# Kernel tuning notes

Measured on AMD Instinct MI355X. Metric: run time of the kernel, lower is better.

The kernel has to match this reference:

```python
import jax, jax.numpy as jnp
import numpy as np

B, T, D, H = 4, 2048, 1024, 16
DH = D // H  # 64


def setup_inputs() -> dict:
    key = jax.random.key(0)
    k1, k2, k3 = jax.random.split(key, 3)
    x = jax.random.normal(k1, (B, T, D), dtype=jnp.float32)
    w_qkv = jax.random.normal(k2, (D, 3 * D), dtype=jnp.float32) * (D ** -0.5)
    w_out = jax.random.normal(k3, (D, D), dtype=jnp.float32) * (D ** -0.5)
    return {"x": x, "w_qkv": w_qkv, "w_out": w_out}


def reference(x, w_qkv, w_out):
    b, t, d = x.shape
    qkv = jnp.einsum('btd,de->bte', x, w_qkv)  # [B,T,3D]
    q, k, v = jnp.split(qkv, 3, axis=-1)
    # [B,H,T,DH]
    q = q.reshape(b, t, H, DH).transpose(0, 2, 1, 3)
    k = k.reshape(b, t, H, DH).transpose(0, 2, 1, 3)
    v = v.reshape(b, t, H, DH).transpose(0, 2, 1, 3)
    logits = jnp.einsum('bhqd,bhkd->bhqk', q, k) * (1.0 / jnp.sqrt(jnp.float32(DH)))
    # causal bias: -inf strictly above the diagonal (key index > query index)
    causal = jnp.tril(jnp.ones((t, t), dtype=bool))
    logits = jnp.where(causal, logits, jnp.float32(-jnp.inf))
    scores = jax.nn.softmax(logits, axis=-1)
    y = jnp.einsum('bhqk,bhkd->bhqd', scores, v)
    y = y.transpose(0, 2, 1, 3).reshape(b, t, d)
    return jnp.einsum('btd,de->bte', y, w_out)
```

## Files before the change

### kernel.cpp

```cpp
#include <hip/hip_runtime.h>
#include <hip/hip_bf16.h>


namespace {
constexpr int kB = 4, kT = 2048, kD = 1024, kH = 16;
constexpr int kM = kB * kT;
constexpr int kNq = 3 * kD;
constexpr float kS = 0.180336880f;
}

typedef unsigned short u16;
typedef short bf16x8 __attribute__((ext_vector_type(8)));
typedef float f32x4 __attribute__((ext_vector_type(4)));

__device__ __forceinline__ u16 f2bf(float f) {
  unsigned int u = __float_as_uint(f);
  u += 0x7fffu + ((u >> 16) & 1u);
  return (u16)(u >> 16);
}
__device__ __forceinline__ unsigned int pack2(float a, float b) {
  return (unsigned int)f2bf(a) | ((unsigned int)f2bf(b) << 16);
}
__device__ __forceinline__ unsigned int cvtpk(float a, float b) {
  unsigned int r;
  asm("v_cvt_pk_bf16_f32 %0, %1, %2" : "=v"(r) : "v"(a), "v"(b));
  return r;
}

__device__ __forceinline__ void gload16(const u16* g, u16* l) {
  __builtin_amdgcn_global_load_lds(
      (const __attribute__((address_space(1))) unsigned int*)(uintptr_t)g,
      (__attribute__((address_space(3))) unsigned int*)(uintptr_t)l, 16, 0, 0);
}

__global__ __launch_bounds__(256) void cvt_bf16(const float* __restrict__ x,
                                                u16* __restrict__ xb) {
  const size_t i = ((size_t)blockIdx.x * 256 + threadIdx.x) * 8;
  const float4 v0 = *(const float4*)(x + i);
  const float4 v1 = *(const float4*)(x + i + 4);
  uint4 p;
  p.x = pack2(v0.x, v0.y);
  p.y = pack2(v0.z, v0.w);
  p.z = pack2(v1.x, v1.y);
  p.w = pack2(v1.z, v1.w);
  *(uint4*)(xb + i) = p;
}

__global__ __launch_bounds__(256) void transpose_bf(const float* __restrict__ W,
                                                    u16* __restrict__ WT,
                                                    int K, int N, int nscale) {
  __shared__ float T[32][33];
  const int tid = threadIdx.x;
  const int nb = blockIdx.x * 32, kb = blockIdx.y * 32;
  const int r = tid >> 3, c = (tid & 7) * 4;
  const float4 v = *(const float4*)&W[(size_t)(kb + r) * N + nb + c];
  T[r][c + 0] = v.x;
  T[r][c + 1] = v.y;
  T[r][c + 2] = v.z;
  T[r][c + 3] = v.w;
  __syncthreads();
  const float s = (nb + r < nscale) ? kS : 1.0f;
  uint2 p;
  p.x = pack2(T[c + 0][r] * s, T[c + 1][r] * s);
  p.y = pack2(T[c + 2][r] * s, T[c + 3][r] * s);
  *(uint2*)&WT[(size_t)(nb + r) * K + kb + c] = p;
}

template <bool F32OUT>
__global__ __launch_bounds__(256) void gemm_bt(const u16* __restrict__ A,
                                               const u16* __restrict__ BT,
                                               void* __restrict__ Cv, int lda,
                                               int ldc) {
  __shared__ u16 As[128 * 32];
  __shared__ u16 Bs[128 * 32];
  const int tid = threadIdx.x;
  const int w = tid >> 6, lane = tid & 63;
  const int col = lane & 15, quad = lane >> 4;
  const int wm = (w & 1) * 64, wn = (w >> 1) * 64;
  const int m0 = blockIdx.y * 128, n0 = blockIdx.x * 128;

  const int s0 = tid, s1 = 256 + tid;
  const int ar0 = s0 >> 2, ak0 = ((s0 & 3) ^ ((ar0 >> 1) & 3)) * 8;
  const int ar1 = s1 >> 2, ak1 = ((s1 & 3) ^ ((ar1 >> 1) & 3)) * 8;
  const u16* agp0 = A + (size_t)(m0 + ar0) * lda + ak0;
  const u16* agp1 = A + (size_t)(m0 + ar1) * lda + ak1;
  const u16* bgp0 = BT + (size_t)(n0 + ar0) * kD + ak0;
  const u16* bgp1 = BT + (size_t)(n0 + ar1) * kD + ak1;
  u16* al0 = &As[s0 * 8];
  u16* al1 = &As[s1 * 8];
  u16* bl0 = &Bs[s0 * 8];
  u16* bl1 = &Bs[s1 * 8];

  f32x4 acc[4][4];
#pragma unroll
  for (int mi = 0; mi < 4; ++mi)
#pragma unroll
    for (int ni = 0; ni < 4; ++ni) acc[mi][ni] = (f32x4){0.f, 0.f, 0.f, 0.f};

  for (int k0 = 0; k0 < kD; k0 += 32) {
    __syncthreads();
    gload16(agp0 + k0, al0);
    gload16(agp1 + k0, al1);
    gload16(bgp0 + k0, bl0);
    gload16(bgp1 + k0, bl1);
    __syncthreads();
    bf16x8 af[4], bfr[4];
#pragma unroll
    for (int mi = 0; mi < 4; ++mi) {
      const int r = wm + mi * 16 + col;
      af[mi] = *(const bf16x8*)&As[r * 32 + ((quad ^ ((r >> 1) & 3)) * 8)];
    }
#pragma unroll
    for (int ni = 0; ni < 4; ++ni) {
      const int r = wn + ni * 16 + col;
      bfr[ni] = *(const bf16x8*)&Bs[r * 32 + ((quad ^ ((r >> 1) & 3)) * 8)];
    }
#pragma unroll
    for (int mi = 0; mi < 4; ++mi)
#pragma unroll
      for (int ni = 0; ni < 4; ++ni)
        acc[mi][ni] = __builtin_amdgcn_mfma_f32_16x16x32_bf16(
            af[mi], bfr[ni], acc[mi][ni], 0, 0, 0);
  }

#pragma unroll
  for (int mi = 0; mi < 4; ++mi)
#pragma unroll
    for (int reg = 0; reg < 4; ++reg) {
      const int row = m0 + wm + mi * 16 + quad * 4 + reg;
#pragma unroll
      for (int ni = 0; ni < 4; ++ni) {
        const int cc = n0 + wn + ni * 16 + col;
        if (F32OUT)
          ((float*)Cv)[(size_t)row * ldc + cc] = acc[mi][ni][reg];
        else
          ((u16*)Cv)[(size_t)row * ldc + cc] = f2bf(acc[mi][ni][reg]);
      }
    }
}

__global__ __launch_bounds__(256) void attn_fwd(u16* __restrict__ qkv) {
  __shared__ u16 Ks[64 * 64];
  __shared__ u16 Vt[64][72];
  __shared__ u16 Ps[64][72];
  const int tid = threadIdx.x;
  const int w = tid >> 6, lane = tid & 63;
  const int col = lane & 15, quad = lane >> 4;
  const int bh = blockIdx.x;
  const int b = bh >> 4, h = bh & 15;
  const int pa = blockIdx.y;
  const size_t base = (size_t)(b * kT) * kNq + h * 64;

  const int krr = lane >> 3;
  const int ksw = (lane & 7) ^ krr;
  const u16* const kgbase =
      qkv + base + kD + (size_t)(w * 16 + krr) * kNq + ksw * 8;
  u16* const kl0 = &Ks[(w * 16) * 64];
  u16* const kl1 = &Ks[(w * 16 + 8) * 64];

  const int vkp = (tid & 31) * 2, vd0 = (tid >> 5) * 8;

#pragma unroll
  for (int pass = 0; pass < 2; ++pass) {
    const int qt = pass ? (31 - pa) : pa;
    const int q0 = qt << 6;

    bf16x8 aq[2];
#pragma unroll
    for (int ks = 0; ks < 2; ++ks)
      aq[ks] = *(const bf16x8*)(qkv + base + (size_t)(q0 + w * 16 + col) * kNq +
                                ks * 32 + quad * 8);

    f32x4 o[4];
#pragma unroll
    for (int nt = 0; nt < 4; ++nt) o[nt] = (f32x4){0.f, 0.f, 0.f, 0.f};
    float l_i = 0.f;

    for (int kt = 0; kt <= qt; ++kt) {
      const int k0 = kt << 6;
      __syncthreads();
      gload16(kgbase + (size_t)k0 * kNq, kl0);
      gload16(kgbase + (size_t)(k0 + 8) * kNq, kl1);
      {
        const u16* vp = qkv + base + 2 * kD + (size_t)(k0 + vkp) * kNq + vd0;
        const uint4 va = *(const uint4*)vp;
        const uint4 vb = *(const uint4*)(vp + kNq);
        const unsigned int* aw = (const unsigned int*)&va;
        const unsigned int* bw = (const unsigned int*)&vb;
#pragma unroll
        for (int i = 0; i < 4; ++i) {
          *(unsigned int*)&Vt[vd0 + 2 * i][vkp] =
              __builtin_amdgcn_perm(bw[i], aw[i], 0x05040100u);
          *(unsigned int*)&Vt[vd0 + 2 * i + 1][vkp] =
              __builtin_amdgcn_perm(bw[i], aw[i], 0x07060302u);
        }
      }
      __syncthreads();

      f32x4 st[4];
#pragma unroll
      for (int nt = 0; nt < 4; ++nt) st[nt] = (f32x4){0.f, 0.f, 0.f, 0.f};
#pragma unroll
      for (int ks = 0; ks < 2; ++ks) {
#pragma unroll
        for (int nt = 0; nt < 4; ++nt) {
          const int kr = nt * 16 + col;
          const bf16x8 bk = *(const bf16x8*)&Ks[kr * 64 +
                                                (((ks * 4 + quad) ^ (col & 7)) *
                                                 8)];
          st[nt] = __builtin_amdgcn_mfma_f32_16x16x32_bf16(bk, aq[ks], st[nt],
                                                           0, 0, 0);
        }
      }

      float psum = 0.f;
      if (kt == qt) {
        const int qrel = w * 16 + col;
#pragma unroll
        for (int nt = 0; nt < 4; ++nt)
#pragma unroll
          for (int reg = 0; reg < 4; ++reg) {
            const int krel = nt * 16 + quad * 4 + reg;
            const float p = (krel <= qrel) ? exp2f(st[nt][reg]) : 0.f;
            st[nt][reg] = p;
            psum += p;
          }
      } else {
#pragma unroll
        for (int nt = 0; nt < 4; ++nt)
#pragma unroll
          for (int reg = 0; reg < 4; ++reg) {
            const float p = exp2f(st[nt][reg]);
            st[nt][reg] = p;
            psum += p;
          }
      }
      psum += __shfl_xor(psum, 16, 64);
      psum += __shfl_xor(psum, 32, 64);
      l_i += psum;

#pragma unroll
      for (int nt = 0; nt < 4; ++nt) {
        uint2 pk;
        pk.x = cvtpk(st[nt][0], st[nt][1]);
        pk.y = cvtpk(st[nt][2], st[nt][3]);
        *(uint2*)&Ps[w * 16 + col][nt * 16 + quad * 4] = pk;
      }

#pragma unroll
      for (int ks = 0; ks < 2; ++ks) {
        const bf16x8 ap =
            *(const bf16x8*)&Ps[w * 16 + col][ks * 32 + quad * 8];
#pragma unroll
        for (int nt = 0; nt < 4; ++nt) {
          const bf16x8 bv =
              *(const bf16x8*)&Vt[nt * 16 + col][ks * 32 + quad * 8];
          o[nt] = __builtin_amdgcn_mfma_f32_16x16x32_bf16(ap, bv, o[nt], 0, 0,
                                                          0);
        }
      }
    }

#pragma unroll
    for (int reg = 0; reg < 4; ++reg) {
      const float lq = __shfl(l_i, (lane & 48) | (quad * 4 + reg), 64);
      const float inv = 1.0f / lq;
      u16* yp =
          qkv + base + (size_t)(q0 + w * 16 + quad * 4 + reg) * kNq;
#pragma unroll
      for (int nt = 0; nt < 4; ++nt)
        yp[nt * 16 + col] = f2bf(o[nt][reg] * inv);
    }
  }
}

extern "C" void kernel_launch(void* const* d_in, const int* in_sizes, int n_in,
                              void* d_out, int out_size, void* d_ws,
                              size_t ws_size, hipStream_t stream) {
  const float* x = (const float*)d_in[0];
  const float* w_qkv = (const float*)d_in[1];
  const float* w_out = (const float*)d_in[2];

  u16* wqkvT = (u16*)d_ws;
  u16* woutT = wqkvT + (size_t)kNq * kD;
  u16* qkvb = woutT + (size_t)kD * kD;
  u16* xb = (u16*)d_out;

  cvt_bf16<<<kM * kD / 2048, 256, 0, stream>>>(x, xb);
  transpose_bf<<<dim3(kNq / 32, kD / 32), 256, 0, stream>>>(w_qkv, wqkvT, kD,
                                                            kNq, kD);
  transpose_bf<<<dim3(kD / 32, kD / 32), 256, 0, stream>>>(w_out, woutT, kD,
                                                           kD, 0);
  gemm_bt<false><<<dim3(kNq / 128, kM / 128), 256, 0, stream>>>(xb, wqkvT,
                                                                qkvb, kD, kNq);
  attn_fwd<<<dim3(kB * kH, 16), 256, 0, stream>>>(qkvb);
  gemm_bt<true><<<dim3(kD / 128, kM / 128), 256, 0, stream>>>(qkvb, woutT,
                                                              d_out, kNq, kD);
}
```

Baseline: 265.9 us.

## Double-buffer K/V tile loads and compute softmax row sums via ones-MFMA

The attention kernel now keeps two K tiles in shared memory and register-prefetches the next V tile. The loads for tile kt+1 are issued right after the barrier, so they overlap the QK and PV MFMAs of tile kt. The row-sum of probabilities moves from scalar adds plus cross-lane shuffles to an extra MFMA against a ones vector, and exp2f becomes the raw hardware exp2 builtin. This costs more shared memory and registers, and the denominator is now summed from the bf16-rounded probabilities.

Result: faster. 250.0 us (-6.0%).

```diff
diff --git a/kernel.cpp b/kernel.cpp
--- a/kernel.cpp
+++ b/kernel.cpp
@@ -140,7 +140,7 @@
 }
 
 __global__ __launch_bounds__(256) void attn_fwd(u16* __restrict__ qkv) {
-  __shared__ u16 Ks[64 * 64];
+  __shared__ u16 Ks[2][64 * 64];
   __shared__ u16 Vt[64][72];
   __shared__ u16 Ps[64][72];
   const int tid = threadIdx.x;
@@ -155,11 +155,15 @@
   const int ksw = (lane & 7) ^ krr;
   const u16* const kgbase =
       qkv + base + kD + (size_t)(w * 16 + krr) * kNq + ksw * 8;
-  u16* const kl0 = &Ks[(w * 16) * 64];
-  u16* const kl1 = &Ks[(w * 16 + 8) * 64];
 
   const int vkp = (tid & 31) * 2, vd0 = (tid >> 5) * 8;
-
+  const u16* const vgbase = qkv + base + 2 * kD + (size_t)vkp * kNq + vd0;
+
+  bf16x8 onesf;
+#pragma unroll
+  for (int i = 0; i < 8; ++i) onesf[i] = (short)0x3F80;
+
+  int cur = 0;
 #pragma unroll
   for (int pass = 0; pass < 2; ++pass) {
     const int qt = pass ? (31 - pa) : pa;
@@ -171,20 +175,19 @@
       aq[ks] = *(const bf16x8*)(qkv + base + (size_t)(q0 + w * 16 + col) * kNq +
                                 ks * 32 + quad * 8);
 
+    gload16(kgbase, &Ks[cur][(w * 16) * 64]);
+    gload16(kgbase + (size_t)8 * kNq, &Ks[cur][(w * 16 + 8) * 64]);
+    uint4 va = *(const uint4*)vgbase;
+    uint4 vb = *(const uint4*)(vgbase + kNq);
+
     f32x4 o[4];
 #pragma unroll
     for (int nt = 0; nt < 4; ++nt) o[nt] = (f32x4){0.f, 0.f, 0.f, 0.f};
-    float l_i = 0.f;
+    f32x4 o4 = (f32x4){0.f, 0.f, 0.f, 0.f};
 
     for (int kt = 0; kt <= qt; ++kt) {
-      const int k0 = kt << 6;
       __syncthreads();
-      gload16(kgbase + (size_t)k0 * kNq, kl0);
-      gload16(kgbase + (size_t)(k0 + 8) * kNq, kl1);
       {
-        const u16* vp = qkv + base + 2 * kD + (size_t)(k0 + vkp) * kNq + vd0;
-        const uint4 va = *(const uint4*)vp;
-        const uint4 vb = *(const uint4*)(vp + kNq);
         const unsigned int* aw = (const unsigned int*)&va;
         const unsigned int* bw = (const unsigned int*)&vb;
 #pragma unroll
@@ -197,6 +200,14 @@
       }
       __syncthreads();
 
+      if (kt < qt) {
+        const size_t ko = (size_t)((kt + 1) << 6) * kNq;
+        gload16(kgbase + ko, &Ks[cur ^ 1][(w * 16) * 64]);
+        gload16(kgbase + ko + (size_t)8 * kNq, &Ks[cur ^ 1][(w * 16 + 8) * 64]);
+        va = *(const uint4*)(vgbase + ko);
+        vb = *(const uint4*)(vgbase + ko + kNq);
+      }
+
       f32x4 st[4];
 #pragma unroll
       for (int nt = 0; nt < 4; ++nt) st[nt] = (f32x4){0.f, 0.f, 0.f, 0.f};
@@ -205,15 +216,15 @@
 #pragma unroll
         for (int nt = 0; nt < 4; ++nt) {
           const int kr = nt * 16 + col;
-          const bf16x8 bk = *(const bf16x8*)&Ks[kr * 64 +
-                                                (((ks * 4 + quad) ^ (col & 7)) *
-                                                 8)];
+          const bf16x8 bk = *(const bf16x8*)&Ks[cur][kr * 64 +
+                                                     (((ks * 4 + quad) ^
+                                                       (col & 7)) *
+                                                      8)];
           st[nt] = __builtin_amdgcn_mfma_f32_16x16x32_bf16(bk, aq[ks], st[nt],
                                                            0, 0, 0);
         }
       }
 
-      float psum = 0.f;
       if (kt == qt) {
         const int qrel = w * 16 + col;
 #pragma unroll
@@ -221,23 +232,16 @@
 #pragma unroll
           for (int reg = 0; reg < 4; ++reg) {
             const int krel = nt * 16 + quad * 4 + reg;
-            const float p = (krel <= qrel) ? exp2f(st[nt][reg]) : 0.f;
-            st[nt][reg] = p;
-            psum += p;
+            st[nt][reg] =
+                (krel <= qrel) ? __builtin_amdgcn_exp2f(st[nt][reg]) : 0.f;
           }
       } else {
 #pragma unroll
         for (int nt = 0; nt < 4; ++nt)
 #pragma unroll
-          for (int reg = 0; reg < 4; ++reg) {
-            const float p = exp2f(st[nt][reg]);
-            st[nt][reg] = p;
-            psum += p;
-          }
-      }
-      psum += __shfl_xor(psum, 16, 64);
-      psum += __shfl_xor(psum, 32, 64);
-      l_i += psum;
+          for (int reg = 0; reg < 4; ++reg)
+            st[nt][reg] = __builtin_amdgcn_exp2f(st[nt][reg]);
+      }
 
 #pragma unroll
       for (int nt = 0; nt < 4; ++nt) {
@@ -258,15 +262,15 @@
           o[nt] = __builtin_amdgcn_mfma_f32_16x16x32_bf16(ap, bv, o[nt], 0, 0,
                                                           0);
         }
-      }
+        o4 = __builtin_amdgcn_mfma_f32_16x16x32_bf16(ap, onesf, o4, 0, 0, 0);
+      }
+      cur ^= 1;
     }
 
 #pragma unroll
     for (int reg = 0; reg < 4; ++reg) {
-      const float lq = __shfl(l_i, (lane & 48) | (quad * 4 + reg), 64);
-      const float inv = 1.0f / lq;
-      u16* yp =
-          qkv + base + (size_t)(q0 + w * 16 + quad * 4 + reg) * kNq;
+      const float inv = 1.0f / o4[reg];
+      u16* yp = qkv + base + (size_t)(q0 + w * 16 + quad * 4 + reg) * kNq;
 #pragma unroll
       for (int nt = 0; nt < 4; ++nt)
         yp[nt * 16 + col] = f2bf(o[nt][reg] * inv);
```
